# Kernel tuning notes

Measured on AMD Instinct MI355X. Metric: run time of the kernel, lower is better.

Reference implementation:

```python
import jax, jax.numpy as jnp
import numpy as np

B, S, H = 8, 2048, 2048

def setup_inputs() -> dict:
    key = jax.random.key(0)
    ks = jax.random.split(key, 7)
    return {
        "time_decay": jax.random.normal(ks[0], (H,), dtype=jnp.float32),
        "key": jax.random.normal(ks[1], (B, S, H), dtype=jnp.float32),
        "time_first": jax.random.normal(ks[2], (H,), dtype=jnp.float32),
        "value": jax.random.normal(ks[3], (B, S, H), dtype=jnp.float32),
        "max_state": jax.random.normal(ks[4], (B, H), dtype=jnp.float32),
        "num_state": jax.random.normal(ks[5], (B, H), dtype=jnp.float32),
        "den_state": jax.random.uniform(ks[6], (B, H), dtype=jnp.float32),
    }

def _wkv(time_decay, k, time_first, v, max_state, num_state, den_state):
    f32 = jnp.float32
    td = -jnp.exp(time_decay.astype(f32))          # [H]
    tf = time_first.astype(f32)                    # [H]
    k = k.astype(f32)
    v = v.astype(f32)

    def step(carry, kv_t):
        m, num, den = carry                        # each [B,H]
        kt, vt = kv_t                              # each [B,H]
        # output branch: include time_first bonus
        mo = jnp.maximum(m, kt + tf)
        e1o = jnp.exp(m - mo)
        e2o = jnp.exp(kt + tf - mo)
        out = (e1o * num + e2o * vt) / (e1o * den + e2o)
        # state branch: apply decay
        ms = jnp.maximum(m + td, kt)
        e1s = jnp.exp(m + td - ms)
        e2s = jnp.exp(kt - ms)
        return (ms, e1s * num + e2s * vt, e1s * den + e2s), out

    carry0 = (max_state.astype(f32), num_state.astype(f32), den_state.astype(f32))
    # scan over time: move seq axis to front -> [S,B,H]
    (m, num, den), outs = jax.lax.scan(
        step, carry0, (jnp.swapaxes(k, 0, 1), jnp.swapaxes(v, 0, 1)))
    output = jnp.swapaxes(outs, 0, 1)              # [B,S,H]
    return output, m, num, den

def reference(time_decay, key, time_first, value, max_state, num_state, den_state):
    return _wkv(time_decay, key, time_first, value, max_state, num_state, den_state)
```

## Files before the change

### kernel.cpp

```cpp
#include <hip/hip_runtime.h>


#ifndef TCH
#define TCH 16
#endif

__device__ __forceinline__ float ex2(float x) { return __builtin_amdgcn_exp2f(x); }
__device__ __forceinline__ float rcpf(float x) { return __builtin_amdgcn_rcpf(x); }

__device__ __forceinline__ float wkv_step(float kts, float vt, float tfs, float tds,
                                          float& m, float& num, float& den)
{
    const float ktf = kts + tfs;
    const float mo  = fmaxf(m, ktf);
    const float e1o = ex2(m - mo);
    const float e2o = ex2(ktf - mo);
    const float o   = (e1o * num + e2o * vt) * rcpf(e1o * den + e2o);
    const float mpd = m + tds;
    const float ms  = fmaxf(mpd, kts);
    const float e1s = ex2(mpd - ms);
    const float e2s = ex2(kts - ms);
    num = e1s * num + e2s * vt;
    den = e1s * den + e2s;
    m   = ms;
    return o;
}

__global__ __launch_bounds__(64, 1)
void wkv_fwd(const float* __restrict__ td_in, const float* __restrict__ kin,
             const float* __restrict__ tf_in, const float* __restrict__ vin,
             const float* __restrict__ m0, const float* __restrict__ n0,
             const float* __restrict__ d0,
             float* __restrict__ out, float* __restrict__ m_out,
             float* __restrict__ n_out, float* __restrict__ dn_out,
             int B, int S, int H)
{
    const int g = blockIdx.x * 64 + threadIdx.x;
    if (g >= B * H) return;
    const int b = g / H;
    const int h = g - b * H;

    constexpr float C  = 1.4426950408889634f;
    constexpr float IC = 0.6931471805599453f;

    const float tds = -ex2(td_in[h] * C) * C;
    const float tfs = tf_in[h] * C;

    float m   = m0[g] * C;
    float num = n0[g];
    float den = d0[g];

    const size_t base = (size_t)b * (size_t)S * (size_t)H + (size_t)h;
    const float* kp = kin + base;
    const float* vp = vin + base;
    float*       op = out + base;

    const int nc = S / TCH;

    float ka[TCH], va[TCH], kb[TCH], vb[TCH];

    if (nc > 0) {
        #pragma unroll
        for (int i = 0; i < TCH; ++i) {
            ka[i] = kp[(size_t)i * H];
            va[i] = vp[(size_t)i * H];
        }
    }

    int t = 0;
    for (int c = 0; c + 2 <= nc; c += 2) {
        #pragma unroll
        for (int i = 0; i < TCH; ++i) {
            kb[i] = kp[(size_t)(t + TCH + i) * H];
            vb[i] = vp[(size_t)(t + TCH + i) * H];
        }
        #pragma unroll
        for (int i = 0; i < TCH; ++i) {
            op[(size_t)(t + i) * H] = wkv_step(ka[i] * C, va[i], tfs, tds, m, num, den);
        }
        t += TCH;
        if (c + 2 < nc) {
            #pragma unroll
            for (int i = 0; i < TCH; ++i) {
                ka[i] = kp[(size_t)(t + TCH + i) * H];
                va[i] = vp[(size_t)(t + TCH + i) * H];
            }
        }
        #pragma unroll
        for (int i = 0; i < TCH; ++i) {
            op[(size_t)(t + i) * H] = wkv_step(kb[i] * C, vb[i], tfs, tds, m, num, den);
        }
        t += TCH;
    }
    if (nc & 1) {
        #pragma unroll
        for (int i = 0; i < TCH; ++i) {
            op[(size_t)(t + i) * H] = wkv_step(ka[i] * C, va[i], tfs, tds, m, num, den);
        }
        t += TCH;
    }
    for (; t < S; ++t) {
        const float kt = kp[(size_t)t * H];
        const float vt = vp[(size_t)t * H];
        op[(size_t)t * H] = wkv_step(kt * C, vt, tfs, tds, m, num, den);
    }

    m_out[g]  = m * IC;
    n_out[g]  = num;
    dn_out[g] = den;
}

extern "C" void kernel_launch(void* const* d_in, const int* in_sizes, int n_in,
                              void* d_out, int out_size, void* d_ws, size_t ws_size,
                              hipStream_t stream)
{
    const float* time_decay = (const float*)d_in[0];
    const float* key        = (const float*)d_in[1];
    const float* time_first = (const float*)d_in[2];
    const float* value      = (const float*)d_in[3];
    const float* max_state  = (const float*)d_in[4];
    const float* num_state  = (const float*)d_in[5];
    const float* den_state  = (const float*)d_in[6];

    const int H  = in_sizes[0];
    const int BH = in_sizes[4];
    const int B  = BH / H;
    const int S  = in_sizes[1] / BH;

    float* out    = (float*)d_out;
    float* m_out  = out + (size_t)B * (size_t)S * (size_t)H;
    float* n_out  = m_out + BH;
    float* dn_out = n_out + BH;

    const int grid = (BH + 63) / 64;
    wkv_fwd<<<grid, 64, 0, stream>>>(time_decay, key, time_first, value,
                                     max_state, num_state, den_state,
                                     out, m_out, n_out, dn_out, B, S, H);
}
```

Measured before the change: 386.5 us.

## Stream key/value chunks into LDS with async global_load_lds double buffering

```diff
diff --git a/kernel.cpp b/kernel.cpp
--- a/kernel.cpp
+++ b/kernel.cpp
@@ -5,8 +5,19 @@
 #define TCH 16
 #endif
 
-__device__ __forceinline__ float ex2(float x) { return __builtin_amdgcn_exp2f(x); }
+#define VM_WAIT0  asm volatile("s_waitcnt vmcnt(0)" ::: "memory")
+#define VM_WAIT16 asm volatile("s_waitcnt vmcnt(16)" ::: "memory")
+#define CFENCE    asm volatile("" ::: "memory")
+
+__device__ __forceinline__ float ex2(float x)  { return __builtin_amdgcn_exp2f(x); }
 __device__ __forceinline__ float rcpf(float x) { return __builtin_amdgcn_rcpf(x); }
+
+__device__ __forceinline__ void gload_lds4(const float* g, float* l) {
+    __builtin_amdgcn_global_load_lds(
+        (const __attribute__((address_space(1))) unsigned int*)g,
+        (__attribute__((address_space(3))) unsigned int*)l,
+        4, 0, 0);
+}
 
 __device__ __forceinline__ float wkv_step(float kts, float vt, float tfs, float tds,
                                           float& m, float& num, float& den)
@@ -35,8 +46,11 @@
              float* __restrict__ n_out, float* __restrict__ dn_out,
              int B, int S, int H)
 {
-    const int g = blockIdx.x * 64 + threadIdx.x;
-    if (g >= B * H) return;
+    __shared__ float lds[2][TCH][2][64];
+
+    const int lane = threadIdx.x;
+    int g = blockIdx.x * 64 + lane;
+    if (g >= B * H) g = B * H - 1;
     const int b = g / H;
     const int h = g - b * H;
 
@@ -56,49 +70,43 @@
     float*       op = out + base;
 
     const int nc = S / TCH;
-
-    float ka[TCH], va[TCH], kb[TCH], vb[TCH];
+    int t = 0;
 
     if (nc > 0) {
+        CFENCE;
         #pragma unroll
         for (int i = 0; i < TCH; ++i) {
-            ka[i] = kp[(size_t)i * H];
-            va[i] = vp[(size_t)i * H];
+            gload_lds4(kp + (size_t)i * H, &lds[0][i][0][0]);
+            gload_lds4(vp + (size_t)i * H, &lds[0][i][1][0]);
+        }
+        CFENCE;
+
+        for (int c = 0; c < nc; ++c) {
+            const int bf = c & 1;
+            if (c == 0) { VM_WAIT0; } else { VM_WAIT16; }
+
+            if (c + 1 < nc) {
+                const int nb = bf ^ 1;
+                const size_t t1 = (size_t)t + TCH;
+                #pragma unroll
+                for (int i = 0; i < TCH; ++i) {
+                    gload_lds4(kp + (t1 + i) * (size_t)H, &lds[nb][i][0][0]);
+                    gload_lds4(vp + (t1 + i) * (size_t)H, &lds[nb][i][1][0]);
+                }
+            }
+            CFENCE;
+
+            #pragma unroll
+            for (int i = 0; i < TCH; ++i) {
+                const float kt = lds[bf][i][0][lane];
+                const float vt = lds[bf][i][1][lane];
+                op[(size_t)(t + i) * H] = wkv_step(kt * C, vt, tfs, tds, m, num, den);
+            }
+            CFENCE;
+            t += TCH;
         }
     }
 
-    int t = 0;
-    for (int c = 0; c + 2 <= nc; c += 2) {
-        #pragma unroll
-        for (int i = 0; i < TCH; ++i) {
-            kb[i] = kp[(size_t)(t + TCH + i) * H];
-            vb[i] = vp[(size_t)(t + TCH + i) * H];
-        }
-        #pragma unroll
-        for (int i = 0; i < TCH; ++i) {
-            op[(size_t)(t + i) * H] = wkv_step(ka[i] * C, va[i], tfs, tds, m, num, den);
-        }
-        t += TCH;
-        if (c + 2 < nc) {
-            #pragma unroll
-            for (int i = 0; i < TCH; ++i) {
-                ka[i] = kp[(size_t)(t + TCH + i) * H];
-                va[i] = vp[(size_t)(t + TCH + i) * H];
-            }
-        }
-        #pragma unroll
-        for (int i = 0; i < TCH; ++i) {
-            op[(size_t)(t + i) * H] = wkv_step(kb[i] * C, vb[i], tfs, tds, m, num, den);
-        }
-        t += TCH;
-    }
-    if (nc & 1) {
-        #pragma unroll
-        for (int i = 0; i < TCH; ++i) {
-            op[(size_t)(t + i) * H] = wkv_step(ka[i] * C, va[i], tfs, tds, m, num, den);
-        }
-        t += TCH;
-    }
     for (; t < S; ++t) {
         const float kt = kp[(size_t)t * H];
         const float vt = vp[(size_t)t * H];
```

New measurement: 485.0 us. 25.5% more time.

## Parallelize time scan within block via segmented prefix combine and LDS DMA

Applied to the files above, without the earlier changes.

```diff
diff --git a/kernel.cpp b/kernel.cpp
--- a/kernel.cpp
+++ b/kernel.cpp
@@ -1,32 +1,24 @@
 #include <hip/hip_runtime.h>
 
 
-#ifndef TCH
-#define TCH 16
-#endif
-
-__device__ __forceinline__ float ex2(float x) { return __builtin_amdgcn_exp2f(x); }
+#define TILE 128
+#define NW   8
+#define SUB  (TILE / NW)
+
+#define VMW0   asm volatile("s_waitcnt vmcnt(0)" ::: "memory")
+#define VMW16  asm volatile("s_waitcnt vmcnt(16)" ::: "memory")
+#define BARR   asm volatile("s_waitcnt lgkmcnt(0)\n\ts_barrier" ::: "memory")
+
+__device__ __forceinline__ float ex2(float x)  { return __builtin_amdgcn_exp2f(x); }
 __device__ __forceinline__ float rcpf(float x) { return __builtin_amdgcn_rcpf(x); }
 
-__device__ __forceinline__ float wkv_step(float kts, float vt, float tfs, float tds,
-                                          float& m, float& num, float& den)
-{
-    const float ktf = kts + tfs;
-    const float mo  = fmaxf(m, ktf);
-    const float e1o = ex2(m - mo);
-    const float e2o = ex2(ktf - mo);
-    const float o   = (e1o * num + e2o * vt) * rcpf(e1o * den + e2o);
-    const float mpd = m + tds;
-    const float ms  = fmaxf(mpd, kts);
-    const float e1s = ex2(mpd - ms);
-    const float e2s = ex2(kts - ms);
-    num = e1s * num + e2s * vt;
-    den = e1s * den + e2s;
-    m   = ms;
-    return o;
-}
-
-__global__ __launch_bounds__(64, 1)
+__device__ __forceinline__ void dma16(const float* g, float* l) {
+    __builtin_amdgcn_global_load_lds(
+        (const __attribute__((address_space(1))) unsigned int*)g,
+        (__attribute__((address_space(3))) unsigned int*)l, 16, 0, 0);
+}
+
+__global__ __launch_bounds__(512)
 void wkv_fwd(const float* __restrict__ td_in, const float* __restrict__ kin,
              const float* __restrict__ tf_in, const float* __restrict__ vin,
              const float* __restrict__ m0, const float* __restrict__ n0,
@@ -35,79 +27,168 @@
              float* __restrict__ n_out, float* __restrict__ dn_out,
              int B, int S, int H)
 {
+    __shared__ float kbuf[2][TILE][64];
+    __shared__ float vbuf[2][TILE][64];
+    __shared__ float smry[NW][3][64];
+    __shared__ float cry[2][3][64];
+
+    const int tid  = threadIdx.x;
+    const int lane = tid & 63;
+    const int w    = tid >> 6;
+
+    const int bpb = H >> 6;
+    const int b   = blockIdx.x / bpb;
+    const int hb  = (blockIdx.x - b * bpb) << 6;
+    const int h   = hb + lane;
+    const int g   = b * H + h;
+
+    constexpr float Cc = 1.4426950408889634f;
+    constexpr float IC = 0.6931471805599453f;
+
+    const float tds  = -ex2(td_in[h] * Cc) * Cc;
+    const float tfs  = tf_in[h] * Cc;
+    const float dseg = tds * (float)SUB;
+
+    if (w == 0) {
+        cry[0][0][lane] = m0[g] * Cc;
+        cry[0][1][lane] = n0[g];
+        cry[0][2][lane] = d0[g];
+    }
+
+    const size_t base = (size_t)b * (size_t)S * (size_t)H + (size_t)hb;
+    const float* gk = kin + base;
+    const float* gv = vin + base;
+    float*       go = out + base;
+
+    const int sub = lane >> 4;
+    const int c4  = (lane & 15) << 2;
+
+    const int ntiles = S / TILE;
+
+    #pragma unroll
+    for (int i = 0; i < 4; ++i) {
+        const int r = w * SUB + i * 4;
+        dma16(gk + (size_t)(r + sub) * H + c4, &kbuf[0][r][0]);
+        dma16(gv + (size_t)(r + sub) * H + c4, &vbuf[0][r][0]);
+    }
+
+    float M = 0.f, N = 0.f, D = 0.f;
+
+    for (int it = 0; it < ntiles; ++it) {
+        const int p = it & 1;
+        if (it == 0) { VMW0; } else { VMW16; }
+        BARR;
+
+        if (it + 1 < ntiles) {
+            const int np = p ^ 1;
+            const size_t t1 = (size_t)(it + 1) * TILE;
+            #pragma unroll
+            for (int i = 0; i < 4; ++i) {
+                const int r = w * SUB + i * 4;
+                dma16(gk + (t1 + r + sub) * (size_t)H + c4, &kbuf[np][r][0]);
+                dma16(gv + (t1 + r + sub) * (size_t)H + c4, &vbuf[np][r][0]);
+            }
+        }
+
+        float lm = -1e30f, ln = 0.f, ldn = 0.f;
+        #pragma unroll
+        for (int j = 0; j < SUB; ++j) {
+            const float kt  = kbuf[p][w * SUB + j][lane] * Cc;
+            const float vt  = vbuf[p][w * SUB + j][lane];
+            const float mpd = lm + tds;
+            const float ms  = fmaxf(mpd, kt);
+            const float e1  = ex2(mpd - ms);
+            const float e2  = ex2(kt - ms);
+            ln  = e1 * ln  + e2 * vt;
+            ldn = e1 * ldn + e2;
+            lm  = ms;
+        }
+        smry[w][0][lane] = lm;
+        smry[w][1][lane] = ln;
+        smry[w][2][lane] = ldn;
+        BARR;
+
+        M = cry[p][0][lane];
+        N = cry[p][1][lane];
+        D = cry[p][2][lane];
+        for (int j = 0; j < w; ++j) {
+            const float Md = M + dseg;
+            const float sm = smry[j][0][lane];
+            const float M2 = fmaxf(Md, sm);
+            const float a  = ex2(Md - M2);
+            const float bb = ex2(sm - M2);
+            N = a * N + bb * smry[j][1][lane];
+            D = a * D + bb * smry[j][2][lane];
+            M = M2;
+        }
+
+        float* po = go + ((size_t)it * TILE + (size_t)w * SUB) * (size_t)H;
+        #pragma unroll
+        for (int j = 0; j < SUB; ++j) {
+            const float kt  = kbuf[p][w * SUB + j][lane] * Cc;
+            const float vt  = vbuf[p][w * SUB + j][lane];
+            const float ktf = kt + tfs;
+            const float mo  = fmaxf(M, ktf);
+            const float e1o = ex2(M - mo);
+            const float e2o = ex2(ktf - mo);
+            po[(size_t)j * H + lane] =
+                (e1o * N + e2o * vt) * rcpf(e1o * D + e2o);
+            const float mpd = M + tds;
+            const float ms  = fmaxf(mpd, kt);
+            const float e1s = ex2(mpd - ms);
+            const float e2s = ex2(kt - ms);
+            N = e1s * N + e2s * vt;
+            D = e1s * D + e2s;
+            M = ms;
+        }
+
+        if (w == NW - 1) {
+            cry[p ^ 1][0][lane] = M;
+            cry[p ^ 1][1][lane] = N;
+            cry[p ^ 1][2][lane] = D;
+        }
+    }
+
+    if (w == NW - 1) {
+        m_out[g]  = M * IC;
+        n_out[g]  = N;
+        dn_out[g] = D;
+    }
+}
+
+__global__ __launch_bounds__(64)
+void wkv_fwd_serial(const float* __restrict__ td_in, const float* __restrict__ kin,
+                    const float* __restrict__ tf_in, const float* __restrict__ vin,
+                    const float* __restrict__ m0, const float* __restrict__ n0,
+                    const float* __restrict__ d0,
+                    float* __restrict__ out, float* __restrict__ m_out,
+                    float* __restrict__ n_out, float* __restrict__ dn_out,
+                    int B, int S, int H)
+{
     const int g = blockIdx.x * 64 + threadIdx.x;
     if (g >= B * H) return;
     const int b = g / H;
     const int h = g - b * H;
-
-    constexpr float C  = 1.4426950408889634f;
-    constexpr float IC = 0.6931471805599453f;
-
-    const float tds = -ex2(td_in[h] * C) * C;
-    const float tfs = tf_in[h] * C;
-
-    float m   = m0[g] * C;
-    float num = n0[g];
-    float den = d0[g];
-
-    const size_t base = (size_t)b * (size_t)S * (size_t)H + (size_t)h;
-    const float* kp = kin + base;
-    const float* vp = vin + base;
-    float*       op = out + base;
-
-    const int nc = S / TCH;
-
-    float ka[TCH], va[TCH], kb[TCH], vb[TCH];
-
-    if (nc > 0) {
-        #pragma unroll
-        for (int i = 0; i < TCH; ++i) {
-            ka[i] = kp[(size_t)i * H];
-            va[i] = vp[(size_t)i * H];
-        }
-    }
-
-    int t = 0;
-    for (int c = 0; c + 2 <= nc; c += 2) {
-        #pragma unroll
-        for (int i = 0; i < TCH; ++i) {
-            kb[i] = kp[(size_t)(t + TCH + i) * H];
-            vb[i] = vp[(size_t)(t + TCH + i) * H];
-        }
-        #pragma unroll
-        for (int i = 0; i < TCH; ++i) {
-            op[(size_t)(t + i) * H] = wkv_step(ka[i] * C, va[i], tfs, tds, m, num, den);
-        }
-        t += TCH;
-        if (c + 2 < nc) {
-            #pragma unroll
-            for (int i = 0; i < TCH; ++i) {
-                ka[i] = kp[(size_t)(t + TCH + i) * H];
-                va[i] = vp[(size_t)(t + TCH + i) * H];
-            }
-        }
-        #pragma unroll
-        for (int i = 0; i < TCH; ++i) {
-            op[(size_t)(t + i) * H] = wkv_step(kb[i] * C, vb[i], tfs, tds, m, num, den);
-        }
-        t += TCH;
-    }
-    if (nc & 1) {
-        #pragma unroll
-        for (int i = 0; i < TCH; ++i) {
-            op[(size_t)(t + i) * H] = wkv_step(ka[i] * C, va[i], tfs, tds, m, num, den);
-        }
-        t += TCH;
-    }
-    for (; t < S; ++t) {
-        const float kt = kp[(size_t)t * H];
-        const float vt = vp[(size_t)t * H];
-        op[(size_t)t * H] = wkv_step(kt * C, vt, tfs, tds, m, num, den);
-    }
-
-    m_out[g]  = m * IC;
-    n_out[g]  = num;
-    dn_out[g] = den;
+    constexpr float Cc = 1.4426950408889634f, IC = 0.6931471805599453f;
+    const float tds = -ex2(td_in[h] * Cc) * Cc;
+    const float tfs = tf_in[h] * Cc;
+    float M = m0[g] * Cc, N = n0[g], D = d0[g];
+    const size_t base = (size_t)b * S * H + h;
+    for (int t = 0; t < S; ++t) {
+        const float kt  = kin[base + (size_t)t * H] * Cc;
+        const float vt  = vin[base + (size_t)t * H];
+        const float ktf = kt + tfs;
+        const float mo  = fmaxf(M, ktf);
+        const float e1o = ex2(M - mo), e2o = ex2(ktf - mo);
+        out[base + (size_t)t * H] = (e1o * N + e2o * vt) * rcpf(e1o * D + e2o);
+        const float mpd = M + tds;
+        const float ms  = fmaxf(mpd, kt);
+        const float e1s = ex2(mpd - ms), e2s = ex2(kt - ms);
+        N = e1s * N + e2s * vt;
+        D = e1s * D + e2s;
+        M = ms;
+    }
+    m_out[g] = M * IC; n_out[g] = N; dn_out[g] = D;
 }
 
 extern "C" void kernel_launch(void* const* d_in, const int* in_sizes, int n_in,
@@ -132,8 +213,15 @@
     float* n_out  = m_out + BH;
     float* dn_out = n_out + BH;
 
-    const int grid = (BH + 63) / 64;
-    wkv_fwd<<<grid, 64, 0, stream>>>(time_decay, key, time_first, value,
-                                     max_state, num_state, den_state,
-                                     out, m_out, n_out, dn_out, B, S, H);
-}
+    if ((H % 64 == 0) && (S % TILE == 0)) {
+        const int grid = BH / 64;
+        wkv_fwd<<<grid, 512, 0, stream>>>(time_decay, key, time_first, value,
+                                          max_state, num_state, den_state,
+                                          out, m_out, n_out, dn_out, B, S, H);
+    } else {
+        const int grid = (BH + 63) / 64;
+        wkv_fwd_serial<<<grid, 64, 0, stream>>>(time_decay, key, time_first, value,
+                                                max_state, num_state, den_state,
+                                                out, m_out, n_out, dn_out, B, S, H);
+    }
+}
```

After: 349.3 us. 1.11x faster.
